# Optimization experiments

Hardware: AMD Instinct MI355X
Metric: run time of the kernel (lower is better)

## Reference

```python
import jax, jax.numpy as jnp
import numpy as np

NUM_HEADS = 12


def setup_inputs() -> dict:
    key = jax.random.key(0)
    k1, k2, k3 = jax.random.split(key, 3)
    B, N, C = 16, 1024, 768
    x = jax.random.normal(k1, (B, N, C), dtype=jnp.float32)
    w_qkv = jax.random.normal(k2, (C, 3 * C), dtype=jnp.float32) * (C ** -0.5)
    w_proj = jax.random.normal(k3, (C, C), dtype=jnp.float32) * (C ** -0.5)
    b_proj = jnp.zeros((C,), dtype=jnp.float32)
    return {"x": x, "w_qkv": w_qkv, "w_proj": w_proj, "b_proj": b_proj}


def reference(x, w_qkv, w_proj, b_proj):
    B, N, C = x.shape
    H = NUM_HEADS
    d = C // H
    scale = d ** -0.5
    # QKV projection (no bias, qkv_bias=False)
    qkv = jnp.einsum('bnc,cf->bnf', x, w_qkv)            # [B, N, 3C]
    qkv = qkv.reshape(B, N, 3, H, d).transpose(2, 0, 3, 1, 4)  # [3, B, H, N, d]
    q, k, v = qkv[0], qkv[1], qkv[2]
    attn = jnp.einsum('bhnd,bhmd->bhnm', q, k) * scale   # [B, H, N, N]
    attn = jax.nn.softmax(attn, axis=-1)
    out = jnp.einsum('bhnm,bhmd->bhnd', attn, v)          # [B, H, N, d]
    # Faithful to source: reshape [B,H,N,d] -> [B,N,H*d] WITHOUT head transpose
    out = out.reshape(B, N, H * d)
    return jnp.einsum('bnc,cf->bnf', out, w_proj) + b_proj
```

## Files before the change

kernel.cpp:

```cpp
#include <hip/hip_runtime.h>
#include <math.h>
#include <cstddef>
#include <cstdint>


typedef _Float16 half8 __attribute__((ext_vector_type(8)));
typedef float f32x4 __attribute__((ext_vector_type(4)));

__device__ __forceinline__ void async_ld16(const void* src, void* lds) {
  __builtin_amdgcn_global_load_lds(
      (const __attribute__((address_space(1))) unsigned int*)src,
      (__attribute__((address_space(3))) unsigned int*)lds, 16, 0, 0);
}

__device__ __forceinline__ f32x4 mfma16(half8 a, half8 b, f32x4 c) {
  return __builtin_amdgcn_mfma_f32_16x16x32_f16(a, b, c, 0, 0, 0);
}

__global__ __launch_bounds__(256) void conv_split(const float* __restrict__ src,
                                                  _Float16* __restrict__ hi,
                                                  _Float16* __restrict__ lo,
                                                  int n8) {
  for (int i = blockIdx.x * blockDim.x + threadIdx.x; i < n8;
       i += gridDim.x * blockDim.x) {
    const float4 f0 = ((const float4*)src)[i * 2];
    const float4 f1 = ((const float4*)src)[i * 2 + 1];
    const float x[8] = {f0.x, f0.y, f0.z, f0.w, f1.x, f1.y, f1.z, f1.w};
    half8 h, l;
#pragma unroll
    for (int j = 0; j < 8; ++j) {
      const _Float16 hv = (_Float16)x[j];
      h[j] = hv;
      l[j] = (_Float16)(x[j] - (float)hv);
    }
    ((half8*)hi)[i] = h;
    ((half8*)lo)[i] = l;
  }
}

__global__ __launch_bounds__(256) void conv_wT(const float* __restrict__ W,
                                               _Float16* __restrict__ Th,
                                               _Float16* __restrict__ Tl,
                                               int K, int N) {
  __shared__ float T[64][65];
  const int n0 = blockIdx.x * 64, k0 = blockIdx.y * 64;
  const int t = threadIdx.x, r = t >> 2, c4 = t & 3;
#pragma unroll
  for (int q = 0; q < 4; ++q) {
    const float4 v = *reinterpret_cast<const float4*>(
        &W[(size_t)(k0 + r) * N + n0 + c4 * 16 + q * 4]);
    T[r][c4 * 16 + q * 4 + 0] = v.x;
    T[r][c4 * 16 + q * 4 + 1] = v.y;
    T[r][c4 * 16 + q * 4 + 2] = v.z;
    T[r][c4 * 16 + q * 4 + 3] = v.w;
  }
  __syncthreads();
  half8 h0, h1, l0, l1;
#pragma unroll
  for (int j = 0; j < 8; ++j) {
    const float x0 = T[c4 * 16 + j][r];
    const _Float16 hv0 = (_Float16)x0;
    h0[j] = hv0; l0[j] = (_Float16)(x0 - (float)hv0);
    const float x1 = T[c4 * 16 + 8 + j][r];
    const _Float16 hv1 = (_Float16)x1;
    h1[j] = hv1; l1[j] = (_Float16)(x1 - (float)hv1);
  }
  const size_t ob = (size_t)(n0 + r) * K + k0 + c4 * 16;
  *(half8*)&Th[ob] = h0;
  *(half8*)&Th[ob + 8] = h1;
  *(half8*)&Tl[ob] = l0;
  *(half8*)&Tl[ob + 8] = l1;
}

template <bool HAS_BIAS>
__global__ __launch_bounds__(256, 2) void gemm_split(
    const _Float16* __restrict__ Ah, const _Float16* __restrict__ Al,
    const _Float16* __restrict__ Bh, const _Float16* __restrict__ Bl,
    const float* __restrict__ bias, float* __restrict__ C,
    int M, int N, int K) {
  __shared__ _Float16 AsH[128 * 64], AsL[128 * 64], BsH[128 * 64], BsL[128 * 64];
  const int tid = threadIdx.x;
  const int w = tid >> 6, l = tid & 63;
  const int kl = l & 15, lgrp = l >> 4;
  const int rl = l >> 3, cl = l & 7;
  const int bm = blockIdx.y * 128, bn = blockIdx.x * 128;
  const int wm = (w & 1) * 64, wn = (w >> 1) * 64;

  f32x4 acc[4][4];
#pragma unroll
  for (int m = 0; m < 4; ++m)
#pragma unroll
    for (int n = 0; n < 4; ++n) acc[m][n] = f32x4{0.f, 0.f, 0.f, 0.f};

  for (int k0 = 0; k0 < K; k0 += 64) {
    __syncthreads();
#pragma unroll
    for (int j = 0; j < 4; ++j) {
      const int rloc = w * 32 + j * 8 + rl;
      const size_t koff = (size_t)k0 + ((cl ^ (rloc & 7)) << 3);
      const int ldsb = (w * 32 + j * 8) * 64;
      async_ld16(Ah + (size_t)(bm + rloc) * K + koff, &AsH[ldsb]);
      async_ld16(Al + (size_t)(bm + rloc) * K + koff, &AsL[ldsb]);
      async_ld16(Bh + (size_t)(bn + rloc) * K + koff, &BsH[ldsb]);
      async_ld16(Bl + (size_t)(bn + rloc) * K + koff, &BsL[ldsb]);
    }
    asm volatile("s_waitcnt vmcnt(0)" ::: "memory");
    __syncthreads();

#pragma unroll
    for (int ks = 0; ks < 2; ++ks) {
      half8 ah[4], al[4], bh[4], bl[4];
#pragma unroll
      for (int m = 0; m < 4; ++m) {
        const int row = wm + m * 16 + kl;
        const int off = row * 64 + (((ks * 4 + lgrp) ^ (row & 7)) << 3);
        ah[m] = *(const half8*)&AsH[off];
        al[m] = *(const half8*)&AsL[off];
      }
#pragma unroll
      for (int n = 0; n < 4; ++n) {
        const int row = wn + n * 16 + kl;
        const int off = row * 64 + (((ks * 4 + lgrp) ^ (row & 7)) << 3);
        bh[n] = *(const half8*)&BsH[off];
        bl[n] = *(const half8*)&BsL[off];
      }
#pragma unroll
      for (int m = 0; m < 4; ++m)
#pragma unroll
        for (int n = 0; n < 4; ++n) {
          acc[m][n] = mfma16(ah[m], bh[n], acc[m][n]);
          acc[m][n] = mfma16(al[m], bh[n], acc[m][n]);
          acc[m][n] = mfma16(ah[m], bl[n], acc[m][n]);
        }
    }
  }

  float bv[4];
  if (HAS_BIAS) {
#pragma unroll
    for (int n = 0; n < 4; ++n) bv[n] = bias[bn + wn + n * 16 + kl];
  }
#pragma unroll
  for (int m = 0; m < 4; ++m)
#pragma unroll
    for (int r = 0; r < 4; ++r) {
      const int row = bm + wm + m * 16 + lgrp * 4 + r;
#pragma unroll
      for (int n = 0; n < 4; ++n) {
        float v = acc[m][n][r];
        if (HAS_BIAS) v += bv[n];
        C[(size_t)row * N + bn + wn + n * 16 + kl] = v;
      }
    }
}

__global__ __launch_bounds__(256) void prep_kv(float* __restrict__ qkv) {
  constexpr int N = 1024, C3 = 2304;
  const int nt = blockIdx.x, h = blockIdx.y, b = blockIdx.z;
  const int t = threadIdx.x;
  __shared__ float Vls[64 * 65];

  const int r = t >> 2, dc = t & 3;
  const size_t rowf = (size_t)(b * N + nt * 64 + r) * C3 + h * 64;

  float kx[16], vx[16];
#pragma unroll
  for (int q = 0; q < 4; ++q) {
    const float4 kv = *reinterpret_cast<const float4*>(&qkv[rowf + 768 + dc * 16 + q * 4]);
    kx[q * 4 + 0] = kv.x; kx[q * 4 + 1] = kv.y; kx[q * 4 + 2] = kv.z; kx[q * 4 + 3] = kv.w;
    const float4 vv = *reinterpret_cast<const float4*>(&qkv[rowf + 1536 + dc * 16 + q * 4]);
    vx[q * 4 + 0] = vv.x; vx[q * 4 + 1] = vv.y; vx[q * 4 + 2] = vv.z; vx[q * 4 + 3] = vv.w;
  }
#pragma unroll
  for (int i = 0; i < 16; ++i) Vls[r * 65 + dc * 16 + i] = vx[i];
  __syncthreads();

  {
    char* base = (char*)qkv + (rowf + 768) * 4;
    half8 h0, h1, l0, l1;
#pragma unroll
    for (int i = 0; i < 8; ++i) {
      const _Float16 hi = (_Float16)kx[i];
      h0[i] = hi; l0[i] = (_Float16)(kx[i] - (float)hi);
      const _Float16 hi2 = (_Float16)kx[i + 8];
      h1[i] = hi2; l1[i] = (_Float16)(kx[i + 8] - (float)hi2);
    }
    *(half8*)(base + dc * 32) = h0;
    *(half8*)(base + dc * 32 + 16) = h1;
    *(half8*)(base + 128 + dc * 32) = l0;
    *(half8*)(base + 128 + dc * 32 + 16) = l1;
  }

#pragma unroll
  for (int p = 0; p < 2; ++p) {
    const int dd = p * 32 + (t >> 3), nc = t & 7;
    half8 hv, lv;
#pragma unroll
    for (int j = 0; j < 8; ++j) {
      const float x = Vls[(nc * 8 + j) * 65 + dd];
      const _Float16 hi = (_Float16)x;
      hv[j] = hi; lv[j] = (_Float16)(x - (float)hi);
    }
    char* vb = (char*)qkv + ((size_t)(b * N + nt * 64 + dd) * C3 + h * 64 + 1536) * 4;
    *(half8*)(vb + nc * 16) = hv;
    *(half8*)(vb + 128 + nc * 16) = lv;
  }
}

__global__ __launch_bounds__(256, 2) void attn_mfma(const float* __restrict__ qkv,
                                                    _Float16* __restrict__ ahi,
                                                    _Float16* __restrict__ alo) {
  constexpr int N = 1024, H = 12, C3 = 2304;
  const int qt = blockIdx.x, h = blockIdx.y, b = blockIdx.z;
  const int tid = threadIdx.x;
  const int w = tid >> 6, l = tid & 63;
  const int kl = l & 15, lgrp = l >> 4;

  __shared__ _Float16 Khi[64 * 64], Klo[64 * 64], Vhi[64 * 64], Vlo[64 * 64];
  __shared__ _Float16 Phi[128 * 64], Plo[128 * 64];

  const int q0 = qt * 128;

  half8 qhi[2][2], qlo[2][2];
#pragma unroll
  for (int qs = 0; qs < 2; ++qs)
#pragma unroll
    for (int ks = 0; ks < 2; ++ks) {
      const float* qp = qkv + (size_t)(b * N + q0 + w * 32 + qs * 16 + kl) * C3 +
                        h * 64 + ks * 32 + lgrp * 8;
      const float4 f0 = *reinterpret_cast<const float4*>(qp);
      const float4 f1 = *reinterpret_cast<const float4*>(qp + 4);
      const float x[8] = {f0.x, f0.y, f0.z, f0.w, f1.x, f1.y, f1.z, f1.w};
#pragma unroll
      for (int j = 0; j < 8; ++j) {
        const float xs = x[j] * 0.125f;
        const _Float16 hi = (_Float16)xs;
        qhi[qs][ks][j] = hi;
        qlo[qs][ks][j] = (_Float16)(xs - (float)hi);
      }
    }

  f32x4 o[2][4];
  float plsum[2][4];
#pragma unroll
  for (int qs = 0; qs < 2; ++qs)
#pragma unroll
    for (int i = 0; i < 4; ++i) {
      plsum[qs][i] = 0.f;
      o[qs][i] = f32x4{0.f, 0.f, 0.f, 0.f};
    }

  const char* qkvB = (const char*)qkv;
  const int rl = l >> 3, cl = l & 7;

  auto stageK = [&](int kb) {
#pragma unroll
    for (int i = 0; i < 2; ++i) {
      const int row = w * 16 + i * 8 + rl;
      const size_t rb = ((size_t)(b * N + kb * 64 + row) * C3 + h * 64) * 4;
      const int sw = (cl ^ (row & 7)) * 16;
      const char* kc = qkvB + rb + 768 * 4 + sw;
      const int lo_ = (w * 16 + i * 8) * 64;
      async_ld16(kc, &Khi[lo_]);
      async_ld16(kc + 128, &Klo[lo_]);
    }
  };
  auto stageV = [&](int kb) {
#pragma unroll
    for (int i = 0; i < 2; ++i) {
      const int row = w * 16 + i * 8 + rl;
      const size_t rb = ((size_t)(b * N + kb * 64 + row) * C3 + h * 64) * 4;
      const int sw = (cl ^ (row & 7)) * 16;
      const char* vc = qkvB + rb + 1536 * 4 + sw;
      const int lo_ = (w * 16 + i * 8) * 64;
      async_ld16(vc, &Vhi[lo_]);
      async_ld16(vc + 128, &Vlo[lo_]);
    }
  };

  stageK(0);
  stageV(0);
  asm volatile("s_waitcnt vmcnt(0)" ::: "memory");
  __builtin_amdgcn_s_barrier();

  for (int kb = 0; kb < 16; ++kb) {
    f32x4 s[2][4];
#pragma unroll
    for (int qs = 0; qs < 2; ++qs)
#pragma unroll
      for (int kt = 0; kt < 4; ++kt) s[qs][kt] = f32x4{0.f, 0.f, 0.f, 0.f};

#pragma unroll
    for (int kt = 0; kt < 4; ++kt)
#pragma unroll
      for (int ks = 0; ks < 2; ++ks) {
        const int rowb = kt * 16 + kl;
        const int off = rowb * 64 + (((ks * 4 + lgrp) ^ (rowb & 7)) << 3);
        const half8 bh = *(const half8*)&Khi[off];
        const half8 bl = *(const half8*)&Klo[off];
#pragma unroll
        for (int qs = 0; qs < 2; ++qs) {
          s[qs][kt] = mfma16(qhi[qs][ks], bh, s[qs][kt]);
          s[qs][kt] = mfma16(qlo[qs][ks], bh, s[qs][kt]);
          s[qs][kt] = mfma16(qhi[qs][ks], bl, s[qs][kt]);
        }
      }

    asm volatile("s_waitcnt vmcnt(0)" ::: "memory");
    __builtin_amdgcn_s_barrier();
    if (kb < 15) stageK(kb + 1);

#pragma unroll
    for (int qs = 0; qs < 2; ++qs)
#pragma unroll
      for (int r = 0; r < 4; ++r) {
        const int prow = w * 32 + qs * 16 + lgrp * 4 + r;
        const int pbase = prow * 64;
        float ps = 0.f;
#pragma unroll
        for (int kt = 0; kt < 4; ++kt) {
          const float p = __expf(s[qs][kt][r]);
          ps += p;
          const _Float16 ph = (_Float16)p;
          const int pidx = pbase + (((kt * 2 + (kl >> 3)) ^ (prow & 7)) << 3) + (kl & 7);
          Phi[pidx] = ph;
          Plo[pidx] = (_Float16)(p - (float)ph);
        }
        plsum[qs][r] += ps;
      }

#pragma unroll
    for (int ks = 0; ks < 2; ++ks) {
      half8 pah[2], pal[2];
#pragma unroll
      for (int qs = 0; qs < 2; ++qs) {
        const int prow = w * 32 + qs * 16 + kl;
        const int off = prow * 64 + (((ks * 4 + lgrp) ^ (prow & 7)) << 3);
        pah[qs] = *(const half8*)&Phi[off];
        pal[qs] = *(const half8*)&Plo[off];
      }
#pragma unroll
      for (int dt = 0; dt < 4; ++dt) {
        const int rowv = dt * 16 + kl;
        const int off = rowv * 64 + (((ks * 4 + lgrp) ^ (rowv & 7)) << 3);
        const half8 vh = *(const half8*)&Vhi[off];
        const half8 vl = *(const half8*)&Vlo[off];
#pragma unroll
        for (int qs = 0; qs < 2; ++qs) {
          o[qs][dt] = mfma16(pah[qs], vh, o[qs][dt]);
          o[qs][dt] = mfma16(pah[qs], vl, o[qs][dt]);
          o[qs][dt] = mfma16(pal[qs], vh, o[qs][dt]);
        }
      }
    }

    __builtin_amdgcn_s_barrier();
    if (kb < 15) {
      stageV(kb + 1);
      asm volatile("s_waitcnt vmcnt(4)" ::: "memory");
    } else {
      asm volatile("s_waitcnt vmcnt(0)" ::: "memory");
    }
    __builtin_amdgcn_s_barrier();
  }

#pragma unroll
  for (int qs = 0; qs < 2; ++qs)
#pragma unroll
    for (int r = 0; r < 4; ++r) {
      float lsum = plsum[qs][r];
#pragma unroll
      for (int ofs = 1; ofs < 16; ofs <<= 1) lsum += __shfl_xor(lsum, ofs);
      const float inv = 1.f / lsum;
      const int qg = q0 + w * 32 + qs * 16 + lgrp * 4 + r;
      const size_t ob = ((size_t)(b * H + h) * N + qg) * 64;
#pragma unroll
      for (int dt = 0; dt < 4; ++dt) {
        const float v = o[qs][dt][r] * inv;
        const _Float16 hv = (_Float16)v;
        ahi[ob + dt * 16 + kl] = hv;
        alo[ob + dt * 16 + kl] = (_Float16)(v - (float)hv);
      }
    }
}

extern "C" void kernel_launch(void* const* d_in, const int* in_sizes, int n_in,
                              void* d_out, int out_size, void* d_ws,
                              size_t ws_size, hipStream_t stream) {
  const float* x = (const float*)d_in[0];
  const float* w_qkv = (const float*)d_in[1];
  const float* w_proj = (const float*)d_in[2];
  const float* b_proj = (const float*)d_in[3];
  float* out = (float*)d_out;

  constexpr int M = 16 * 1024;
  constexpr int C = 768;
  constexpr int C3 = 2304;

  char* wsp = (char*)d_ws;
  float* qkv = (float*)wsp;
  _Float16* xhi = (_Float16*)(wsp + (size_t)M * C3 * 4);
  _Float16* xlo = xhi + (size_t)M * C;
  _Float16* wqh = xlo + (size_t)M * C;
  _Float16* wql = wqh + (size_t)C3 * C;
  _Float16* wph = wql + (size_t)C3 * C;
  _Float16* wpl = wph + (size_t)C * C;
  _Float16* ahi = xhi;
  _Float16* alo = xlo;

  conv_split<<<2048, 256, 0, stream>>>(x, xhi, xlo, M * C / 8);
  conv_wT<<<dim3(C3 / 64, C / 64), 256, 0, stream>>>(w_qkv, wqh, wql, C, C3);
  conv_wT<<<dim3(C / 64, C / 64), 256, 0, stream>>>(w_proj, wph, wpl, C, C);

  gemm_split<false><<<dim3(C3 / 128, M / 128), 256, 0, stream>>>(
      xhi, xlo, wqh, wql, nullptr, qkv, M, C3, C);

  prep_kv<<<dim3(16, 12, 16), 256, 0, stream>>>(qkv);

  attn_mfma<<<dim3(8, 12, 16), 256, 0, stream>>>(qkv, ahi, alo);

  gemm_split<true><<<dim3(C / 128, M / 128), 256, 0, stream>>>(
      ahi, alo, wph, wpl, b_proj, out, M, C, C);
}
```

Baseline: 548.0 us.

## Permute V key order to allow vectorized P stores and XCD-aware block mapping

Permutes the key order of V during prep so that each lane's four softmax probabilities can be written to LDS as one contiguous half4 store instead of four scattered scalar stores. The P read path drops its XOR swizzle to match. The attention grid is flattened to 1D and remapped so that blocks on the same XCD share (batch, head) pairs, improving L2 reuse of K/V. The risks are LDS bank conflicts on the unswizzled P reads and getting the key permutation wrong, which would break correctness.

```diff
diff --git a/kernel.cpp b/kernel.cpp
--- a/kernel.cpp
+++ b/kernel.cpp
@@ -5,6 +5,7 @@
 
 
 typedef _Float16 half8 __attribute__((ext_vector_type(8)));
+typedef _Float16 half4 __attribute__((ext_vector_type(4)));
 typedef float f32x4 __attribute__((ext_vector_type(4)));
 
 __device__ __forceinline__ void async_ld16(const void* src, void* lds) {
@@ -197,7 +198,9 @@
     half8 hv, lv;
 #pragma unroll
     for (int j = 0; j < 8; ++j) {
-      const float x = Vls[(nc * 8 + j) * 65 + dd];
+      const int pos = nc * 8 + j;
+      const int kap = ((pos & 3) << 4) | (pos >> 2);
+      const float x = Vls[kap * 65 + dd];
       const _Float16 hi = (_Float16)x;
       hv[j] = hi; lv[j] = (_Float16)(x - (float)hi);
     }
@@ -211,7 +214,14 @@
                                                     _Float16* __restrict__ ahi,
                                                     _Float16* __restrict__ alo) {
   constexpr int N = 1024, H = 12, C3 = 2304;
-  const int qt = blockIdx.x, h = blockIdx.y, b = blockIdx.z;
+  const int blk = blockIdx.x;
+  const int xcd = blk & 7;
+  const int slot = blk >> 3;
+  const int qt = slot & 7;
+  const int bh = xcd * 24 + (slot >> 3);
+  const int h = bh % H;
+  const int b = bh / H;
+
   const int tid = threadIdx.x;
   const int w = tid >> 6, l = tid & 63;
   const int kl = l & 15, lgrp = l >> 4;
@@ -296,13 +306,13 @@
       for (int ks = 0; ks < 2; ++ks) {
         const int rowb = kt * 16 + kl;
         const int off = rowb * 64 + (((ks * 4 + lgrp) ^ (rowb & 7)) << 3);
-        const half8 bh = *(const half8*)&Khi[off];
-        const half8 bl = *(const half8*)&Klo[off];
+        const half8 bh_ = *(const half8*)&Khi[off];
+        const half8 bl_ = *(const half8*)&Klo[off];
 #pragma unroll
         for (int qs = 0; qs < 2; ++qs) {
-          s[qs][kt] = mfma16(qhi[qs][ks], bh, s[qs][kt]);
-          s[qs][kt] = mfma16(qlo[qs][ks], bh, s[qs][kt]);
-          s[qs][kt] = mfma16(qhi[qs][ks], bl, s[qs][kt]);
+          s[qs][kt] = mfma16(qhi[qs][ks], bh_, s[qs][kt]);
+          s[qs][kt] = mfma16(qlo[qs][ks], bh_, s[qs][kt]);
+          s[qs][kt] = mfma16(qhi[qs][ks], bl_, s[qs][kt]);
         }
       }
 
@@ -315,17 +325,18 @@
 #pragma unroll
       for (int r = 0; r < 4; ++r) {
         const int prow = w * 32 + qs * 16 + lgrp * 4 + r;
-        const int pbase = prow * 64;
         float ps = 0.f;
+        half4 ph4, pl4;
 #pragma unroll
         for (int kt = 0; kt < 4; ++kt) {
           const float p = __expf(s[qs][kt][r]);
           ps += p;
           const _Float16 ph = (_Float16)p;
-          const int pidx = pbase + (((kt * 2 + (kl >> 3)) ^ (prow & 7)) << 3) + (kl & 7);
-          Phi[pidx] = ph;
-          Plo[pidx] = (_Float16)(p - (float)ph);
+          ph4[kt] = ph;
+          pl4[kt] = (_Float16)(p - (float)ph);
         }
+        *(half4*)&Phi[prow * 64 + kl * 4] = ph4;
+        *(half4*)&Plo[prow * 64 + kl * 4] = pl4;
         plsum[qs][r] += ps;
       }
 
@@ -334,8 +345,7 @@
       half8 pah[2], pal[2];
 #pragma unroll
       for (int qs = 0; qs < 2; ++qs) {
-        const int prow = w * 32 + qs * 16 + kl;
-        const int off = prow * 64 + (((ks * 4 + lgrp) ^ (prow & 7)) << 3);
+        const int off = (w * 32 + qs * 16 + kl) * 64 + ks * 32 + lgrp * 8;
         pah[qs] = *(const half8*)&Phi[off];
         pal[qs] = *(const half8*)&Plo[off];
       }
@@ -417,7 +427,7 @@
 
   prep_kv<<<dim3(16, 12, 16), 256, 0, stream>>>(qkv);
 
-  attn_mfma<<<dim3(8, 12, 16), 256, 0, stream>>>(qkv, ahi, alo);
+  attn_mfma<<<1536, 256, 0, stream>>>(qkv, ahi, alo);
 
   gemm_split<true><<<dim3(C / 128, M / 128), 256, 0, stream>>>(
       ahi, alo, wph, wpl, b_proj, out, M, C, C);
```

Result: no change. 537.6 us (-1.9%).
